# Kernel tuning notes

Hardware: AMD Instinct MI355X
Metric: run time of the kernel (lower is better)

Reference implementation:

```python
import jax, jax.numpy as jnp
import numpy as np

WIN = 9
EPS = 1e-05


def _box_w(x, win):
    k = jnp.ones((1, 1, 1, win), x.dtype)
    return jax.lax.conv_general_dilated(
        x, k, window_strides=(1, 1), padding=((0, 0), (win // 2, win // 2)),
        dimension_numbers=('NCHW', 'OIHW', 'NCHW'))


def setup_inputs() -> dict:
    key = jax.random.key(0)
    k1, k2 = jax.random.split(key)
    I = jax.random.normal(k1, (16, 1, 1024, 1024), dtype=jnp.float32)
    J = jax.random.normal(k2, (16, 1, 1024, 1024), dtype=jnp.float32)
    return {"I": I, "J": J}


def reference(I, J):
    win = WIN
    I2 = I * I
    J2 = J * J
    IJ = I * J
    I_sum = _box_w(I, win)
    J_sum = _box_w(J, win)
    I2_sum = _box_w(I2, win)
    J2_sum = _box_w(J2, win)
    IJ_sum = _box_w(IJ, win)
    u_I = I_sum / win
    u_J = J_sum / win
    cross = IJ_sum - u_J * I_sum - u_I * J_sum + u_I * u_J * win
    I_var = I2_sum - 2.0 * u_I * I_sum + u_I * u_I * win
    J_var = J2_sum - 2.0 * u_J * J_sum + u_J * u_J * win
    cc = cross * cross / (I_var * J_var + EPS)
    return -1.0 * jnp.mean(cc) + 1.0
```

## Files before the change

kernel.cpp:

```cpp
#include <hip/hip_runtime.h>

#define W      1024
#define NROWS  16384
#define NPIX   16777216.0
#define EPSF   1e-5f
#define PX     16
#define RPW    2
#define NWAVES (NROWS / RPW)
#define NBLOCKS (NWAVES / 4)

struct Quad { float4 q0, q1, q2, q3; };

__device__ __forceinline__ float row_cc(const Quad& A, const Quad& B, int lane) {
    float4 AL, AR, BL, BR;
    AL.x = __shfl_up(A.q3.x, 1, 64); AL.y = __shfl_up(A.q3.y, 1, 64);
    AL.z = __shfl_up(A.q3.z, 1, 64); AL.w = __shfl_up(A.q3.w, 1, 64);
    BL.x = __shfl_up(B.q3.x, 1, 64); BL.y = __shfl_up(B.q3.y, 1, 64);
    BL.z = __shfl_up(B.q3.z, 1, 64); BL.w = __shfl_up(B.q3.w, 1, 64);
    AR.x = __shfl_down(A.q0.x, 1, 64); AR.y = __shfl_down(A.q0.y, 1, 64);
    AR.z = __shfl_down(A.q0.z, 1, 64); AR.w = __shfl_down(A.q0.w, 1, 64);
    BR.x = __shfl_down(B.q0.x, 1, 64); BR.y = __shfl_down(B.q0.y, 1, 64);
    BR.z = __shfl_down(B.q0.z, 1, 64); BR.w = __shfl_down(B.q0.w, 1, 64);
    if (lane == 0)  { AL = make_float4(0.f,0.f,0.f,0.f); BL = make_float4(0.f,0.f,0.f,0.f); }
    if (lane == 63) { AR = make_float4(0.f,0.f,0.f,0.f); BR = make_float4(0.f,0.f,0.f,0.f); }

    float a[24], b[24];
    a[0]=AL.x; a[1]=AL.y; a[2]=AL.z; a[3]=AL.w;
    a[4]=A.q0.x; a[5]=A.q0.y; a[6]=A.q0.z; a[7]=A.q0.w;
    a[8]=A.q1.x; a[9]=A.q1.y; a[10]=A.q1.z; a[11]=A.q1.w;
    a[12]=A.q2.x; a[13]=A.q2.y; a[14]=A.q2.z; a[15]=A.q2.w;
    a[16]=A.q3.x; a[17]=A.q3.y; a[18]=A.q3.z; a[19]=A.q3.w;
    a[20]=AR.x; a[21]=AR.y; a[22]=AR.z; a[23]=AR.w;
    b[0]=BL.x; b[1]=BL.y; b[2]=BL.z; b[3]=BL.w;
    b[4]=B.q0.x; b[5]=B.q0.y; b[6]=B.q0.z; b[7]=B.q0.w;
    b[8]=B.q1.x; b[9]=B.q1.y; b[10]=B.q1.z; b[11]=B.q1.w;
    b[12]=B.q2.x; b[13]=B.q2.y; b[14]=B.q2.z; b[15]=B.q2.w;
    b[16]=B.q3.x; b[17]=B.q3.y; b[18]=B.q3.z; b[19]=B.q3.w;
    b[20]=BR.x; b[21]=BR.y; b[22]=BR.z; b[23]=BR.w;

    float sAc = 0.f, sBc = 0.f, sAA = 0.f, sBB = 0.f, sAB = 0.f;
#pragma unroll
    for (int k = 0; k < 9; ++k) {
        sAc += a[k];
        sBc += b[k];
        sAA = fmaf(a[k], a[k], sAA);
        sBB = fmaf(b[k], b[k], sBB);
        sAB = fmaf(a[k], b[k], sAB);
    }

    const float ninv = -(1.f / 9.f);
    float acc = 0.f;
#pragma unroll
    for (int p = 0; p < PX; ++p) {
        const float cross = fmaf(sAc * sBc, ninv, sAB);
        const float varA  = fmaf(sAc * sAc, ninv, sAA);
        const float varB  = fmaf(sBc * sBc, ninv, sBB);
        const float denom = fmaf(varA, varB, EPSF);
        acc += (cross * cross) * __builtin_amdgcn_rcpf(denom);
        if (p < PX - 1) {
            const float an = a[9 + p], ao = a[p];
            const float bn = b[9 + p], bo = b[p];
            sAc += an - ao;
            sBc += bn - bo;
            sAA = fmaf(an, an, sAA); sAA = fmaf(ao, -ao, sAA);
            sBB = fmaf(bn, bn, sBB); sBB = fmaf(bo, -bo, sBB);
            sAB = fmaf(an, bn, sAB); sAB = fmaf(ao, -bo, sAB);
        }
    }
    return acc;
}

__global__ __launch_bounds__(256, 4) void lncc_rows(const float* __restrict__ I,
                                                    const float* __restrict__ J,
                                                    float* __restrict__ partials) {
    const int lane = threadIdx.x & 63;
    const int wid  = (blockIdx.x << 2) | (threadIdx.x >> 6);
    const size_t base0 = (size_t)(2 * wid)     * W + lane * PX;
    const size_t base1 = (size_t)(2 * wid + 1) * W + lane * PX;

    Quad A0, B0, A1, B1;
    A0.q0 = *(const float4*)(I + base0);
    A0.q1 = *(const float4*)(I + base0 + 4);
    A0.q2 = *(const float4*)(I + base0 + 8);
    A0.q3 = *(const float4*)(I + base0 + 12);
    B0.q0 = *(const float4*)(J + base0);
    B0.q1 = *(const float4*)(J + base0 + 4);
    B0.q2 = *(const float4*)(J + base0 + 8);
    B0.q3 = *(const float4*)(J + base0 + 12);
    A1.q0 = *(const float4*)(I + base1);
    A1.q1 = *(const float4*)(I + base1 + 4);
    A1.q2 = *(const float4*)(I + base1 + 8);
    A1.q3 = *(const float4*)(I + base1 + 12);
    B1.q0 = *(const float4*)(J + base1);
    B1.q1 = *(const float4*)(J + base1 + 4);
    B1.q2 = *(const float4*)(J + base1 + 8);
    B1.q3 = *(const float4*)(J + base1 + 12);
    __builtin_amdgcn_sched_barrier(0);

    float acc = row_cc(A0, B0, lane);
    __builtin_amdgcn_sched_barrier(0);
    acc     += row_cc(A1, B1, lane);

#pragma unroll
    for (int off = 32; off > 0; off >>= 1)
        acc += __shfl_down(acc, off, 64);
    if (lane == 0) partials[wid] = acc;
}

__global__ __launch_bounds__(256) void lncc_finalize(const float* __restrict__ partials,
                                                     float* __restrict__ out) {
    __shared__ double sh[256];
    const int t = threadIdx.x;
    double s = 0.0;
#pragma unroll
    for (int c = 0; c < 8; ++c) {
        const float4 v = *(const float4*)(partials + (size_t)t * 32 + c * 4);
        s += ((double)v.x + (double)v.y) + ((double)v.z + (double)v.w);
    }
    sh[t] = s;
    __syncthreads();
#pragma unroll
    for (int off = 128; off > 0; off >>= 1) {
        if (t < off) sh[t] += sh[t + off];
        __syncthreads();
    }
    if (t == 0) out[0] = (float)(1.0 - sh[0] / NPIX);
}

extern "C" void kernel_launch(void* const* d_in, const int* in_sizes, int n_in,
                              void* d_out, int out_size, void* d_ws, size_t ws_size,
                              hipStream_t stream) {
    const float* I = (const float*)d_in[0];
    const float* J = (const float*)d_in[1];
    float* partials = (float*)d_ws;
    float* out      = (float*)d_out;

    lncc_rows<<<NBLOCKS, 256, 0, stream>>>(I, J, partials);
    lncc_finalize<<<1, 256, 0, stream>>>(partials, out);
}
```

Baseline: 28.24 us.

## Double-buffer row loads with inline-asm loads and manual vmcnt waits, four rows per wave

Each wave now processes four rows instead of two. Row loads are issued with inline-asm global_load_dwordx4 into two register buffers, and explicit s_waitcnt vmcnt waits let the next row's loads stay in flight while the current row is computed. The finalize kernel is adjusted for half as many partials. The intended gain is overlap of memory latency with compute inside a wave, at the cost of more registers and a lower occupancy hint (launch bounds 2 instead of 4), and fewer waves overall.

```diff
diff --git a/kernel.cpp b/kernel.cpp
--- a/kernel.cpp
+++ b/kernel.cpp
@@ -5,38 +5,66 @@
 #define NPIX   16777216.0
 #define EPSF   1e-5f
 #define PX     16
-#define RPW    2
+#define RPW    4
 #define NWAVES (NROWS / RPW)
 #define NBLOCKS (NWAVES / 4)
 
-struct Quad { float4 q0, q1, q2, q3; };
+typedef float f32x4 __attribute__((ext_vector_type(4)));
 
-__device__ __forceinline__ float row_cc(const Quad& A, const Quad& B, int lane) {
-    float4 AL, AR, BL, BR;
-    AL.x = __shfl_up(A.q3.x, 1, 64); AL.y = __shfl_up(A.q3.y, 1, 64);
-    AL.z = __shfl_up(A.q3.z, 1, 64); AL.w = __shfl_up(A.q3.w, 1, 64);
-    BL.x = __shfl_up(B.q3.x, 1, 64); BL.y = __shfl_up(B.q3.y, 1, 64);
-    BL.z = __shfl_up(B.q3.z, 1, 64); BL.w = __shfl_up(B.q3.w, 1, 64);
-    AR.x = __shfl_down(A.q0.x, 1, 64); AR.y = __shfl_down(A.q0.y, 1, 64);
-    AR.z = __shfl_down(A.q0.z, 1, 64); AR.w = __shfl_down(A.q0.w, 1, 64);
-    BR.x = __shfl_down(B.q0.x, 1, 64); BR.y = __shfl_down(B.q0.y, 1, 64);
-    BR.z = __shfl_down(B.q0.z, 1, 64); BR.w = __shfl_down(B.q0.w, 1, 64);
-    if (lane == 0)  { AL = make_float4(0.f,0.f,0.f,0.f); BL = make_float4(0.f,0.f,0.f,0.f); }
-    if (lane == 63) { AR = make_float4(0.f,0.f,0.f,0.f); BR = make_float4(0.f,0.f,0.f,0.f); }
+#define LOAD8(pi, pj, a0, a1, a2, a3, b0, b1, b2, b3)                  \
+    asm volatile(                                                      \
+        "global_load_dwordx4 %0, %8, off\n\t"                          \
+        "global_load_dwordx4 %1, %8, off offset:16\n\t"                \
+        "global_load_dwordx4 %2, %8, off offset:32\n\t"                \
+        "global_load_dwordx4 %3, %8, off offset:48\n\t"                \
+        "global_load_dwordx4 %4, %9, off\n\t"                          \
+        "global_load_dwordx4 %5, %9, off offset:16\n\t"                \
+        "global_load_dwordx4 %6, %9, off offset:32\n\t"                \
+        "global_load_dwordx4 %7, %9, off offset:48\n\t"                \
+        : "=&v"(a0), "=&v"(a1), "=&v"(a2), "=&v"(a3),                  \
+          "=&v"(b0), "=&v"(b1), "=&v"(b2), "=&v"(b3)                   \
+        : "v"(pi), "v"(pj)                                             \
+        : "memory")
+
+#define RELEASE8(N, a0, a1, a2, a3, b0, b1, b2, b3)                    \
+    do {                                                               \
+        asm volatile("s_waitcnt vmcnt(" #N ")"                         \
+                     : "+v"(a0), "+v"(a1), "+v"(a2), "+v"(a3),         \
+                       "+v"(b0), "+v"(b1), "+v"(b2), "+v"(b3)          \
+                     :: "memory");                                     \
+        __builtin_amdgcn_sched_barrier(0);                             \
+    } while (0)
+
+__device__ __forceinline__ float row_cc(f32x4 A0, f32x4 A1, f32x4 A2, f32x4 A3,
+                                        f32x4 B0, f32x4 B1, f32x4 B2, f32x4 B3,
+                                        int lane) {
+    float AL[4], AR[4], BL[4], BR[4];
+#pragma unroll
+    for (int i = 0; i < 4; ++i) {
+        AL[i] = __shfl_up(A3[i], 1, 64);
+        BL[i] = __shfl_up(B3[i], 1, 64);
+        AR[i] = __shfl_down(A0[i], 1, 64);
+        BR[i] = __shfl_down(B0[i], 1, 64);
+    }
+    if (lane == 0) {
+#pragma unroll
+        for (int i = 0; i < 4; ++i) { AL[i] = 0.f; BL[i] = 0.f; }
+    }
+    if (lane == 63) {
+#pragma unroll
+        for (int i = 0; i < 4; ++i) { AR[i] = 0.f; BR[i] = 0.f; }
+    }
 
     float a[24], b[24];
-    a[0]=AL.x; a[1]=AL.y; a[2]=AL.z; a[3]=AL.w;
-    a[4]=A.q0.x; a[5]=A.q0.y; a[6]=A.q0.z; a[7]=A.q0.w;
-    a[8]=A.q1.x; a[9]=A.q1.y; a[10]=A.q1.z; a[11]=A.q1.w;
-    a[12]=A.q2.x; a[13]=A.q2.y; a[14]=A.q2.z; a[15]=A.q2.w;
-    a[16]=A.q3.x; a[17]=A.q3.y; a[18]=A.q3.z; a[19]=A.q3.w;
-    a[20]=AR.x; a[21]=AR.y; a[22]=AR.z; a[23]=AR.w;
-    b[0]=BL.x; b[1]=BL.y; b[2]=BL.z; b[3]=BL.w;
-    b[4]=B.q0.x; b[5]=B.q0.y; b[6]=B.q0.z; b[7]=B.q0.w;
-    b[8]=B.q1.x; b[9]=B.q1.y; b[10]=B.q1.z; b[11]=B.q1.w;
-    b[12]=B.q2.x; b[13]=B.q2.y; b[14]=B.q2.z; b[15]=B.q2.w;
-    b[16]=B.q3.x; b[17]=B.q3.y; b[18]=B.q3.z; b[19]=B.q3.w;
-    b[20]=BR.x; b[21]=BR.y; b[22]=BR.z; b[23]=BR.w;
+#pragma unroll
+    for (int i = 0; i < 4; ++i) {
+        a[i]      = AL[i];   b[i]      = BL[i];
+        a[4 + i]  = A0[i];   b[4 + i]  = B0[i];
+        a[8 + i]  = A1[i];   b[8 + i]  = B1[i];
+        a[12 + i] = A2[i];   b[12 + i] = B2[i];
+        a[16 + i] = A3[i];   b[16 + i] = B3[i];
+        a[20 + i] = AR[i];   b[20 + i] = BR[i];
+    }
 
     float sAc = 0.f, sBc = 0.f, sAA = 0.f, sBB = 0.f, sAB = 0.f;
 #pragma unroll
@@ -70,36 +98,38 @@
     return acc;
 }
 
-__global__ __launch_bounds__(256, 4) void lncc_rows(const float* __restrict__ I,
+__global__ __launch_bounds__(256, 2) void lncc_rows(const float* __restrict__ I,
                                                     const float* __restrict__ J,
                                                     float* __restrict__ partials) {
     const int lane = threadIdx.x & 63;
     const int wid  = (blockIdx.x << 2) | (threadIdx.x >> 6);
-    const size_t base0 = (size_t)(2 * wid)     * W + lane * PX;
-    const size_t base1 = (size_t)(2 * wid + 1) * W + lane * PX;
+    const size_t base = (size_t)wid * RPW * W + (size_t)lane * PX;
+    const float* pI0 = I + base;
+    const float* pJ0 = J + base;
 
-    Quad A0, B0, A1, B1;
-    A0.q0 = *(const float4*)(I + base0);
-    A0.q1 = *(const float4*)(I + base0 + 4);
-    A0.q2 = *(const float4*)(I + base0 + 8);
-    A0.q3 = *(const float4*)(I + base0 + 12);
-    B0.q0 = *(const float4*)(J + base0);
-    B0.q1 = *(const float4*)(J + base0 + 4);
-    B0.q2 = *(const float4*)(J + base0 + 8);
-    B0.q3 = *(const float4*)(J + base0 + 12);
-    A1.q0 = *(const float4*)(I + base1);
-    A1.q1 = *(const float4*)(I + base1 + 4);
-    A1.q2 = *(const float4*)(I + base1 + 8);
-    A1.q3 = *(const float4*)(I + base1 + 12);
-    B1.q0 = *(const float4*)(J + base1);
-    B1.q1 = *(const float4*)(J + base1 + 4);
-    B1.q2 = *(const float4*)(J + base1 + 8);
-    B1.q3 = *(const float4*)(J + base1 + 12);
+    f32x4 xA0, xA1, xA2, xA3, xB0, xB1, xB2, xB3;
+    f32x4 yA0, yA1, yA2, yA3, yB0, yB1, yB2, yB3;
+
+    LOAD8(pI0,     pJ0,     xA0, xA1, xA2, xA3, xB0, xB1, xB2, xB3);
+    LOAD8(pI0 + W, pJ0 + W, yA0, yA1, yA2, yA3, yB0, yB1, yB2, yB3);
+
+    RELEASE8(8, xA0, xA1, xA2, xA3, xB0, xB1, xB2, xB3);
+    float acc = row_cc(xA0, xA1, xA2, xA3, xB0, xB1, xB2, xB3, lane);
+
     __builtin_amdgcn_sched_barrier(0);
+    LOAD8(pI0 + 2 * W, pJ0 + 2 * W, xA0, xA1, xA2, xA3, xB0, xB1, xB2, xB3);
 
-    float acc = row_cc(A0, B0, lane);
+    RELEASE8(8, yA0, yA1, yA2, yA3, yB0, yB1, yB2, yB3);
+    acc += row_cc(yA0, yA1, yA2, yA3, yB0, yB1, yB2, yB3, lane);
+
     __builtin_amdgcn_sched_barrier(0);
-    acc     += row_cc(A1, B1, lane);
+    LOAD8(pI0 + 3 * W, pJ0 + 3 * W, yA0, yA1, yA2, yA3, yB0, yB1, yB2, yB3);
+
+    RELEASE8(8, xA0, xA1, xA2, xA3, xB0, xB1, xB2, xB3);
+    acc += row_cc(xA0, xA1, xA2, xA3, xB0, xB1, xB2, xB3, lane);
+
+    RELEASE8(0, yA0, yA1, yA2, yA3, yB0, yB1, yB2, yB3);
+    acc += row_cc(yA0, yA1, yA2, yA3, yB0, yB1, yB2, yB3, lane);
 
 #pragma unroll
     for (int off = 32; off > 0; off >>= 1)
@@ -113,8 +143,8 @@
     const int t = threadIdx.x;
     double s = 0.0;
 #pragma unroll
-    for (int c = 0; c < 8; ++c) {
-        const float4 v = *(const float4*)(partials + (size_t)t * 32 + c * 4);
+    for (int c = 0; c < 4; ++c) {
+        const float4 v = *(const float4*)(partials + (size_t)t * 16 + c * 4);
         s += ((double)v.x + (double)v.y) + ((double)v.z + (double)v.w);
     }
     sh[t] = s;
```

Result: slower. 29.91 us (+5.9%).
